# Kernel tuning notes

Hardware: AMD Instinct MI355X
Metric: run time of the kernel (lower is better)

The kernel has to match this reference:

```python
import jax, jax.numpy as jnp
import numpy as np

E, T, D, H = 4, 4096, 2048, 8192

def setup_inputs() -> dict:
    key = jax.random.key(0)
    k1, k2, k3 = jax.random.split(key, 3)
    x = jax.random.normal(k1, (E, T, D), dtype=jnp.float32)
    fc1_w = jax.random.normal(k2, (E, D, H), dtype=jnp.float32) * 0.001
    fc2_w = jax.random.normal(k3, (E, H, D), dtype=jnp.float32) * 0.001
    fc1_b = jnp.zeros((E, 1, H), dtype=jnp.float32)
    fc2_b = jnp.zeros((E, 1, D), dtype=jnp.float32)
    return {"x": x, "fc1_w": fc1_w, "fc1_b": fc1_b, "fc2_w": fc2_w, "fc2_b": fc2_b}

def reference(x, fc1_w, fc1_b, fc2_w, fc2_b):
    # batched expert FFN: y = relu(x @ W1 + b1) @ W2 + b2, per expert e
    y = jnp.einsum('etd,edh->eth', x, fc1_w) + fc1_b
    y = jax.nn.relu(y)
    y = jnp.einsum('eth,ehd->etd', y, fc2_w) + fc2_b
    return y
```

## Files before the change

kernel.cpp:

```cpp
#include <hip/hip_runtime.h>
#include <hip/hip_bf16.h>
#include <stdint.h>

#define E_ 4
#define T_ 4096
#define D_ 2048
#define H_ 8192

typedef __attribute__((ext_vector_type(8))) short bf16x8;
typedef __attribute__((ext_vector_type(4))) float f32x4;
typedef __attribute__((ext_vector_type(4))) unsigned short u16x4;

__device__ __forceinline__ unsigned short f2bf(float f) {
    unsigned int u = __float_as_uint(f);
    u = u + 0x7fffu + ((u >> 16) & 1u);
    return (unsigned short)(u >> 16);
}

__device__ __forceinline__ void async16(const unsigned short* g, unsigned short* l) {
    auto gp = (const __attribute__((address_space(1))) unsigned int*)g;
    auto lp = (__attribute__((address_space(3))) unsigned int*)l;
    __builtin_amdgcn_global_load_lds(gp, lp, 16, 0, 0);
}

__device__ __forceinline__ f32x4 mfma16(bf16x8 a, bf16x8 b, f32x4 c) {
    return __builtin_amdgcn_mfma_f32_16x16x32_bf16(a, b, c, 0, 0, 0);
}

__global__ void cvt_x_kernel(const float4* __restrict__ in, uint2* __restrict__ out, long n4) {
    long i = (long)blockIdx.x * blockDim.x + threadIdx.x;
    long stride = (long)gridDim.x * blockDim.x;
    for (; i < n4; i += stride) {
        float4 v = in[i];
        uint2 o;
        o.x = (unsigned)f2bf(v.x) | ((unsigned)f2bf(v.y) << 16);
        o.y = (unsigned)f2bf(v.z) | ((unsigned)f2bf(v.w) << 16);
        out[i] = o;
    }
}

__global__ void transpose_cvt_kernel(const float* __restrict__ W, unsigned short* __restrict__ Wt,
                                     int R, int C) {
    __shared__ float tile[64][65];
    const float* Wp = W + (size_t)blockIdx.z * R * C;
    unsigned short* Wtp = Wt + (size_t)blockIdx.z * R * C;
    const int c0 = blockIdx.x * 64, r0 = blockIdx.y * 64;
    const int tc = threadIdx.x & 63;
    const int tr = threadIdx.x >> 6;
#pragma unroll
    for (int i = 0; i < 16; ++i) {
        int r = tr * 16 + i;
        tile[r][tc] = Wp[(size_t)(r0 + r) * C + c0 + tc];
    }
    __syncthreads();
#pragma unroll
    for (int i = 0; i < 16; ++i) {
        int r = tr * 16 + i;
        Wtp[(size_t)(c0 + r) * R + r0 + tc] = f2bf(tile[tc][r]);
    }
}

template <int K, int OUT_MODE>
__global__ __launch_bounds__(512, 2) void gemm256_kernel(
    const unsigned short* __restrict__ A,
    const unsigned short* __restrict__ Bt,
    const float* __restrict__ bias,
    void* __restrict__ Cout,
    int M, int N)
{
    constexpr int BK = 64;
    constexpr int NT = K / BK;
    __shared__ __align__(16) unsigned short L[2][2][2][128][64];

    const int nx = gridDim.x, ny = gridDim.y;
    const int nwg = nx * ny * gridDim.z;
    const int w = (blockIdx.z * ny + blockIdx.y) * nx + blockIdx.x;
    const int cpx = nwg >> 3;
    const int xcd = w & 7;
    const int c = w >> 3;
    const int CR = cpx / nx;
    const int GX = (nx % 16 == 0) ? 16 : nx;
    const int g = c / (GX * CR);
    const int r1 = c - g * (GX * CR);
    const int byl = r1 / GX;
    const int bxi = r1 - byl * GX;
    const int fy = xcd * CR + byl;
    const int bx = g * GX + bxi;
    const int e = fy / ny;
    const int by = fy - e * ny;

    const unsigned short* Ae = A + (size_t)e * M * K;
    const unsigned short* Be = Bt + (size_t)e * N * K;
    const int bm0 = by * 256;
    const int bn0 = bx * 256;

    const int tid = threadIdx.x;
    const int lane = tid & 63;
    const int wid = tid >> 6;
    const int wr = wid >> 2;
    const int wc = wid & 3;

    const int srow8 = wid * 8 + (lane >> 3);
    const int skel = 8 * ((lane & 7) ^ (lane >> 3));
    const unsigned short* Abase = Ae + (size_t)(bm0 + srow8) * K + skel;
    const unsigned short* Bbase = Be + (size_t)(bn0 + srow8) * K + skel;

#define STG_A(S_, T_, H_, RO_) \
    async16(Abase + ((size_t)((H_) * 128 + (RO_)) * K + (T_) * BK), \
            &L[S_][0][H_][(RO_) + wid * 8][0])
#define STG_B(S_, T_, H_, RO_) \
    async16(Bbase + ((size_t)((H_) * 128 + (RO_)) * K + (T_) * BK), \
            &L[S_][1][H_][(RO_) + wid * 8][0])

    const int fr = lane & 15;
    const int kq = lane >> 4;
    const int ksw = (lane & 7) << 3;
    const int bh = wc >> 1;
    const int brb = (wc & 1) * 64;

#define RD_A(S_, MOFF_) \
    _Pragma("unroll") for (int m = 0; m < 4; ++m) \
    _Pragma("unroll") for (int kk = 0; kk < 2; ++kk) \
        a[m][kk] = *(const bf16x8*)&L[S_][0][wr][(m + (MOFF_)) * 16 + fr][(kk * 32 + kq * 8) ^ ksw]
#define RD_B(S_, N0_, N1_) \
    _Pragma("unroll") for (int n = (N0_); n < (N1_); ++n) \
    _Pragma("unroll") for (int kk = 0; kk < 2; ++kk) \
        b[n][kk] = *(const bf16x8*)&L[S_][1][bh][brb + n * 16 + fr][(kk * 32 + kq * 8) ^ ksw]

#define MIDBAR do { __builtin_amdgcn_sched_barrier(0); __builtin_amdgcn_s_barrier(); } while (0)
#define CLOSEBAR do { __builtin_amdgcn_s_barrier(); __builtin_amdgcn_sched_barrier(0); } while (0)
#define MFMA_Q(MB_, NB_) do { __builtin_amdgcn_s_setprio(1); \
    _Pragma("unroll") for (int m = 0; m < 4; ++m) \
    _Pragma("unroll") for (int n = 0; n < 2; ++n) \
    _Pragma("unroll") for (int kk = 0; kk < 2; ++kk) \
        acc[(MB_) + m][(NB_) + n] = mfma16(a[m][kk], b[(NB_) + n][kk], acc[(MB_) + m][(NB_) + n]); \
    __builtin_amdgcn_s_setprio(0); } while (0)

    f32x4 acc[8][4] = {};
    bf16x8 a[4][2], b[4][2];

    STG_A(0, 0, 0, 0);  STG_A(0, 0, 1, 0);
    STG_B(0, 0, 0, 0);  STG_B(0, 0, 0, 64);
    STG_B(0, 0, 1, 0);  STG_B(0, 0, 1, 64);
    STG_A(0, 0, 0, 64); STG_A(0, 0, 1, 64);
    STG_A(1, 1, 0, 0);  STG_A(1, 1, 1, 0);
    STG_B(1, 1, 0, 0);  STG_B(1, 1, 0, 64);
    STG_B(1, 1, 1, 0);  STG_B(1, 1, 1, 64);
    asm volatile("s_waitcnt vmcnt(6)" ::: "memory");
    __builtin_amdgcn_sched_barrier(0);
    __builtin_amdgcn_s_barrier();

#define ITER(NOTLAST_) do { \
        const int tA = 2 * j, tB = tA + 1; \
         \
        RD_B(0, 0, 2); RD_A(0, 0); \
        STG_A(1, tB, 0, 64); STG_A(1, tB, 1, 64); \
        MIDBAR; MFMA_Q(0, 0); CLOSEBAR; \
         \
        RD_B(0, 2, 4); \
        if (NOTLAST_) { STG_A(0, tA + 2, 0, 0); STG_A(0, tA + 2, 1, 0); } \
        MIDBAR; MFMA_Q(0, 2); CLOSEBAR; \
         \
        RD_A(0, 4); \
        if (NOTLAST_) { STG_B(0, tA + 2, 0, 0); STG_B(0, tA + 2, 0, 64); } \
        MIDBAR; MFMA_Q(4, 0); CLOSEBAR; \
         \
        if (NOTLAST_) { STG_B(0, tA + 2, 1, 0); STG_B(0, tA + 2, 1, 64); } \
        MIDBAR; MFMA_Q(4, 2); \
        if (NOTLAST_) { asm volatile("s_waitcnt vmcnt(6)" ::: "memory"); } \
        else         { asm volatile("s_waitcnt vmcnt(0)" ::: "memory"); } \
        __builtin_amdgcn_sched_barrier(0); \
        CLOSEBAR; \
         \
        RD_B(1, 0, 2); RD_A(1, 0); \
        if (NOTLAST_) { STG_A(0, tA + 2, 0, 64); STG_A(0, tA + 2, 1, 64); } \
        MIDBAR; MFMA_Q(0, 0); CLOSEBAR; \
         \
        RD_B(1, 2, 4); \
        if (NOTLAST_) { STG_A(1, tB + 2, 0, 0); STG_A(1, tB + 2, 1, 0); } \
        MIDBAR; MFMA_Q(0, 2); CLOSEBAR; \
         \
        RD_A(1, 4); \
        if (NOTLAST_) { STG_B(1, tB + 2, 0, 0); STG_B(1, tB + 2, 0, 64); } \
        MIDBAR; MFMA_Q(4, 0); CLOSEBAR; \
         \
        if (NOTLAST_) { STG_B(1, tB + 2, 1, 0); STG_B(1, tB + 2, 1, 64); } \
        MIDBAR; MFMA_Q(4, 2); \
        if (NOTLAST_) { asm volatile("s_waitcnt vmcnt(6)" ::: "memory"); } \
        else         { asm volatile("s_waitcnt vmcnt(0)" ::: "memory"); } \
        __builtin_amdgcn_sched_barrier(0); \
        CLOSEBAR; \
    } while (0)

    for (int j = 0; j < NT / 2 - 1; ++j) { ITER(true); }
    { const int j = NT / 2 - 1; ITER(false); }

#undef ITER
#undef MFMA_Q
#undef MIDBAR
#undef CLOSEBAR
#undef RD_A
#undef RD_B
#undef STG_A
#undef STG_B

    constexpr int ST = 260;
    float* S = (float*)&L[0][0][0][0][0];
    const int rowq = (lane >> 4) * 4;
    const float* bp = bias + (size_t)e * N;
    const float4 bb4 = *(const float4*)(bp + bn0 + lane * 4);

    unsigned short* Y = (unsigned short*)Cout + (size_t)e * M * N;
    float* O = (float*)Cout + (size_t)e * M * N;

#pragma unroll
    for (int sg = 0; sg < 8; ++sg) {
        __syncthreads();
        if (wr == (sg >> 2)) {
            const int sl = sg & 3;
#pragma unroll
            for (int mm = 0; mm < 2; ++mm) {
#pragma unroll
                for (int n = 0; n < 4; ++n) {
#pragma unroll
                    for (int j2 = 0; j2 < 4; ++j2) {
                        S[(mm * 16 + rowq + j2) * ST + wc * 64 + n * 16 + fr] =
                            acc[2 * sl + mm][n][j2];
                    }
                }
            }
        }
        __syncthreads();
#pragma unroll
        for (int rr = 0; rr < 4; ++rr) {
            const int rl = wid * 4 + rr;
            const int rg = bm0 + sg * 32 + rl;
            f32x4 v = *(const f32x4*)&S[rl * ST + lane * 4];
            v[0] += bb4.x; v[1] += bb4.y; v[2] += bb4.z; v[3] += bb4.w;
            if (OUT_MODE == 0) {
                u16x4 o;
                o[0] = f2bf(fmaxf(v[0], 0.0f));
                o[1] = f2bf(fmaxf(v[1], 0.0f));
                o[2] = f2bf(fmaxf(v[2], 0.0f));
                o[3] = f2bf(fmaxf(v[3], 0.0f));
                *(u16x4*)(Y + (size_t)rg * N + bn0 + lane * 4) = o;
            } else {
                *(f32x4*)(O + (size_t)rg * N + bn0 + lane * 4) = v;
            }
        }
    }
}

extern "C" void kernel_launch(void* const* d_in, const int* in_sizes, int n_in,
                              void* d_out, int out_size, void* d_ws, size_t ws_size,
                              hipStream_t stream) {
    const float* x     = (const float*)d_in[0];
    const float* fc1_w = (const float*)d_in[1];
    const float* fc1_b = (const float*)d_in[2];
    const float* fc2_w = (const float*)d_in[3];
    const float* fc2_b = (const float*)d_in[4];
    float* out = (float*)d_out;

    const size_t n_x  = (size_t)E_ * T_ * D_;
    const size_t n_w1 = (size_t)E_ * D_ * H_;
    const size_t n_w2 = (size_t)E_ * H_ * D_;
    const size_t n_y1 = (size_t)E_ * T_ * H_;

    const size_t need = (n_x + n_w1 + n_w2 + n_y1) * sizeof(unsigned short);
    if (ws_size < need) return;

    unsigned short* xb  = (unsigned short*)d_ws;
    unsigned short* w1t = xb + n_x;
    unsigned short* w2t = w1t + n_w1;
    unsigned short* y1  = w2t + n_w2;

    cvt_x_kernel<<<2048, 256, 0, stream>>>((const float4*)x, (uint2*)xb, (long)(n_x / 4));
    {
        dim3 g(H_ / 64, D_ / 64, E_);
        transpose_cvt_kernel<<<g, 256, 0, stream>>>(fc1_w, w1t, D_, H_);
    }
    {
        dim3 g(D_ / 64, H_ / 64, E_);
        transpose_cvt_kernel<<<g, 256, 0, stream>>>(fc2_w, w2t, H_, D_);
    }
    {
        dim3 g(H_ / 256, T_ / 256, E_);
        gemm256_kernel<D_, 0><<<g, 512, 0, stream>>>(xb, w1t, fc1_b, (void*)y1, T_, H_);
    }
    {
        dim3 g(D_ / 256, T_ / 256, E_);
        gemm256_kernel<H_, 1><<<g, 512, 0, stream>>>(y1, w2t, fc2_b, (void*)out, T_, D_);
    }
}
```

Measured before the change: 1.128 ms.

## Remove mid-phase barriers and overlap LDS fragment reads with MFMA phases

Drops the barrier that sat between each phase's LDS reads and its MFMA block, keeping only the closing barrier. The next phase's B or A fragment reads are moved to run alongside the current MFMA quarter, with the first B read hoisted before the loop. This halves the workgroup barriers per phase and hides LDS latency behind matrix math. The cost is more registers for the fragments and a tighter correctness dependence on barrier placement, since fragment reads now happen right after the vmcnt wait before the closing barrier.

```diff
diff --git a/kernel.cpp b/kernel.cpp
--- a/kernel.cpp
+++ b/kernel.cpp
@@ -127,7 +127,6 @@
     _Pragma("unroll") for (int kk = 0; kk < 2; ++kk) \
         b[n][kk] = *(const bf16x8*)&L[S_][1][bh][brb + n * 16 + fr][(kk * 32 + kq * 8) ^ ksw]
 
-#define MIDBAR do { __builtin_amdgcn_sched_barrier(0); __builtin_amdgcn_s_barrier(); } while (0)
 #define CLOSEBAR do { __builtin_amdgcn_s_barrier(); __builtin_amdgcn_sched_barrier(0); } while (0)
 #define MFMA_Q(MB_, NB_) do { __builtin_amdgcn_s_setprio(1); \
     _Pragma("unroll") for (int m = 0; m < 4; ++m) \
@@ -149,46 +148,61 @@
     asm volatile("s_waitcnt vmcnt(6)" ::: "memory");
     __builtin_amdgcn_sched_barrier(0);
     __builtin_amdgcn_s_barrier();
+    RD_B(0, 0, 2);
 
 #define ITER(NOTLAST_) do { \
         const int tA = 2 * j, tB = tA + 1; \
          \
-        RD_B(0, 0, 2); RD_A(0, 0); \
+        RD_A(0, 0); \
         STG_A(1, tB, 0, 64); STG_A(1, tB, 1, 64); \
-        MIDBAR; MFMA_Q(0, 0); CLOSEBAR; \
-         \
+        __builtin_amdgcn_sched_barrier(0); \
+        MFMA_Q(0, 0); \
         RD_B(0, 2, 4); \
+        CLOSEBAR; \
+         \
         if (NOTLAST_) { STG_A(0, tA + 2, 0, 0); STG_A(0, tA + 2, 1, 0); } \
-        MIDBAR; MFMA_Q(0, 2); CLOSEBAR; \
-         \
+        __builtin_amdgcn_sched_barrier(0); \
+        MFMA_Q(0, 2); \
         RD_A(0, 4); \
+        CLOSEBAR; \
+         \
         if (NOTLAST_) { STG_B(0, tA + 2, 0, 0); STG_B(0, tA + 2, 0, 64); } \
-        MIDBAR; MFMA_Q(4, 0); CLOSEBAR; \
+        __builtin_amdgcn_sched_barrier(0); \
+        MFMA_Q(4, 0); \
+        CLOSEBAR; \
          \
         if (NOTLAST_) { STG_B(0, tA + 2, 1, 0); STG_B(0, tA + 2, 1, 64); } \
-        MIDBAR; MFMA_Q(4, 2); \
         if (NOTLAST_) { asm volatile("s_waitcnt vmcnt(6)" ::: "memory"); } \
         else         { asm volatile("s_waitcnt vmcnt(0)" ::: "memory"); } \
         __builtin_amdgcn_sched_barrier(0); \
-        CLOSEBAR; \
-         \
-        RD_B(1, 0, 2); RD_A(1, 0); \
+        RD_B(1, 0, 2); \
+        MFMA_Q(4, 2); \
+        CLOSEBAR; \
+         \
+        RD_A(1, 0); \
         if (NOTLAST_) { STG_A(0, tA + 2, 0, 64); STG_A(0, tA + 2, 1, 64); } \
-        MIDBAR; MFMA_Q(0, 0); CLOSEBAR; \
-         \
+        __builtin_amdgcn_sched_barrier(0); \
+        MFMA_Q(0, 0); \
         RD_B(1, 2, 4); \
+        CLOSEBAR; \
+         \
         if (NOTLAST_) { STG_A(1, tB + 2, 0, 0); STG_A(1, tB + 2, 1, 0); } \
-        MIDBAR; MFMA_Q(0, 2); CLOSEBAR; \
-         \
+        __builtin_amdgcn_sched_barrier(0); \
+        MFMA_Q(0, 2); \
         RD_A(1, 4); \
+        CLOSEBAR; \
+         \
         if (NOTLAST_) { STG_B(1, tB + 2, 0, 0); STG_B(1, tB + 2, 0, 64); } \
-        MIDBAR; MFMA_Q(4, 0); CLOSEBAR; \
+        __builtin_amdgcn_sched_barrier(0); \
+        MFMA_Q(4, 0); \
+        CLOSEBAR; \
          \
         if (NOTLAST_) { STG_B(1, tB + 2, 1, 0); STG_B(1, tB + 2, 1, 64); } \
-        MIDBAR; MFMA_Q(4, 2); \
         if (NOTLAST_) { asm volatile("s_waitcnt vmcnt(6)" ::: "memory"); } \
         else         { asm volatile("s_waitcnt vmcnt(0)" ::: "memory"); } \
         __builtin_amdgcn_sched_barrier(0); \
+        if (NOTLAST_) { RD_B(0, 0, 2); } \
+        MFMA_Q(4, 2); \
         CLOSEBAR; \
     } while (0)
 
@@ -197,7 +211,6 @@
 
 #undef ITER
 #undef MFMA_Q
-#undef MIDBAR
 #undef CLOSEBAR
 #undef RD_A
 #undef RD_B
```

Result: faster. 1.076 ms (-4.6%).

## Collapse GEMM main loop into two-phase-per-tile schedule with fewer barriers

Applied to the files above, without the earlier changes.

Replaces the eight quarter-phase loop body (16 block barriers per two K-tiles) with two half-phases per tile. Each half-phase issues a full 4x4 MFMA block while the LDS fragments for the next half or next tile are read. All loads for tile T+2 are issued together before the second half. The aim is to cut barrier and s_waitcnt stalls and to overlap LDS reads with MFMA work. In exchange, more A/B fragments and in-flight loads stay live at once, which raises register pressure, and the deeper interleaving carries a risk of LDS read/write hazards.

```diff
diff --git a/kernel.cpp b/kernel.cpp
--- a/kernel.cpp
+++ b/kernel.cpp
@@ -122,18 +122,17 @@
     _Pragma("unroll") for (int m = 0; m < 4; ++m) \
     _Pragma("unroll") for (int kk = 0; kk < 2; ++kk) \
         a[m][kk] = *(const bf16x8*)&L[S_][0][wr][(m + (MOFF_)) * 16 + fr][(kk * 32 + kq * 8) ^ ksw]
-#define RD_B(S_, N0_, N1_) \
-    _Pragma("unroll") for (int n = (N0_); n < (N1_); ++n) \
+#define RD_B(S_) \
+    _Pragma("unroll") for (int n = 0; n < 4; ++n) \
     _Pragma("unroll") for (int kk = 0; kk < 2; ++kk) \
         b[n][kk] = *(const bf16x8*)&L[S_][1][bh][brb + n * 16 + fr][(kk * 32 + kq * 8) ^ ksw]
 
-#define MIDBAR do { __builtin_amdgcn_sched_barrier(0); __builtin_amdgcn_s_barrier(); } while (0)
 #define CLOSEBAR do { __builtin_amdgcn_s_barrier(); __builtin_amdgcn_sched_barrier(0); } while (0)
-#define MFMA_Q(MB_, NB_) do { __builtin_amdgcn_s_setprio(1); \
+#define MFMA_H(MB_) do { __builtin_amdgcn_s_setprio(1); \
     _Pragma("unroll") for (int m = 0; m < 4; ++m) \
-    _Pragma("unroll") for (int n = 0; n < 2; ++n) \
+    _Pragma("unroll") for (int n = 0; n < 4; ++n) \
     _Pragma("unroll") for (int kk = 0; kk < 2; ++kk) \
-        acc[(MB_) + m][(NB_) + n] = mfma16(a[m][kk], b[(NB_) + n][kk], acc[(MB_) + m][(NB_) + n]); \
+        acc[(MB_) + m][n] = mfma16(a[m][kk], b[n][kk], acc[(MB_) + m][n]); \
     __builtin_amdgcn_s_setprio(0); } while (0)
 
     f32x4 acc[8][4] = {};
@@ -149,55 +148,49 @@
     asm volatile("s_waitcnt vmcnt(6)" ::: "memory");
     __builtin_amdgcn_sched_barrier(0);
     __builtin_amdgcn_s_barrier();
-
-#define ITER(NOTLAST_) do { \
-        const int tA = 2 * j, tB = tA + 1; \
-         \
-        RD_B(0, 0, 2); RD_A(0, 0); \
-        STG_A(1, tB, 0, 64); STG_A(1, tB, 1, 64); \
-        MIDBAR; MFMA_Q(0, 0); CLOSEBAR; \
-         \
-        RD_B(0, 2, 4); \
-        if (NOTLAST_) { STG_A(0, tA + 2, 0, 0); STG_A(0, tA + 2, 1, 0); } \
-        MIDBAR; MFMA_Q(0, 2); CLOSEBAR; \
-         \
-        RD_A(0, 4); \
-        if (NOTLAST_) { STG_B(0, tA + 2, 0, 0); STG_B(0, tA + 2, 0, 64); } \
-        MIDBAR; MFMA_Q(4, 0); CLOSEBAR; \
-         \
-        if (NOTLAST_) { STG_B(0, tA + 2, 1, 0); STG_B(0, tA + 2, 1, 64); } \
-        MIDBAR; MFMA_Q(4, 2); \
-        if (NOTLAST_) { asm volatile("s_waitcnt vmcnt(6)" ::: "memory"); } \
-        else         { asm volatile("s_waitcnt vmcnt(0)" ::: "memory"); } \
+    RD_B(0);
+    RD_A(0, 0);
+
+#define PH_A(T_, S_, HAS_NEXT_) do { \
+        if (HAS_NEXT_) { STG_A((S_) ^ 1, (T_) + 1, 0, 64); STG_A((S_) ^ 1, (T_) + 1, 1, 64); } \
         __builtin_amdgcn_sched_barrier(0); \
-        CLOSEBAR; \
-         \
-        RD_B(1, 0, 2); RD_A(1, 0); \
-        if (NOTLAST_) { STG_A(0, tA + 2, 0, 64); STG_A(0, tA + 2, 1, 64); } \
-        MIDBAR; MFMA_Q(0, 0); CLOSEBAR; \
-         \
-        RD_B(1, 2, 4); \
-        if (NOTLAST_) { STG_A(1, tB + 2, 0, 0); STG_A(1, tB + 2, 1, 0); } \
-        MIDBAR; MFMA_Q(0, 2); CLOSEBAR; \
-         \
-        RD_A(1, 4); \
-        if (NOTLAST_) { STG_B(1, tB + 2, 0, 0); STG_B(1, tB + 2, 0, 64); } \
-        MIDBAR; MFMA_Q(4, 0); CLOSEBAR; \
-         \
-        if (NOTLAST_) { STG_B(1, tB + 2, 1, 0); STG_B(1, tB + 2, 1, 64); } \
-        MIDBAR; MFMA_Q(4, 2); \
-        if (NOTLAST_) { asm volatile("s_waitcnt vmcnt(6)" ::: "memory"); } \
-        else         { asm volatile("s_waitcnt vmcnt(0)" ::: "memory"); } \
-        __builtin_amdgcn_sched_barrier(0); \
+        MFMA_H(0); \
+        RD_A(S_, 4); \
         CLOSEBAR; \
     } while (0)
 
-    for (int j = 0; j < NT / 2 - 1; ++j) { ITER(true); }
-    { const int j = NT / 2 - 1; ITER(false); }
-
-#undef ITER
-#undef MFMA_Q
-#undef MIDBAR
+#define PH_B(T_, S_, HAS_NEXT_, HAS_NEXT2_) do { \
+        if (HAS_NEXT2_) { \
+            STG_A(S_, (T_) + 2, 0, 0);  STG_A(S_, (T_) + 2, 1, 0); \
+            STG_B(S_, (T_) + 2, 0, 0);  STG_B(S_, (T_) + 2, 0, 64); \
+            STG_B(S_, (T_) + 2, 1, 0);  STG_B(S_, (T_) + 2, 1, 64); \
+        } \
+        if (HAS_NEXT2_) { asm volatile("s_waitcnt vmcnt(6)" ::: "memory"); } \
+        else            { asm volatile("s_waitcnt vmcnt(0)" ::: "memory"); } \
+        __builtin_amdgcn_sched_barrier(0); \
+        MFMA_H(4); \
+        if (HAS_NEXT_) { RD_B((S_) ^ 1); RD_A((S_) ^ 1, 0); } \
+        CLOSEBAR; \
+    } while (0)
+
+    for (int j = 0; j < NT / 2 - 1; ++j) {
+        const int tA = 2 * j, tB = tA + 1;
+        PH_A(tA, 0, true);
+        PH_B(tA, 0, true, (tA + 2 < NT));
+        PH_A(tB, 1, (tB + 1 < NT));
+        PH_B(tB, 1, (tB + 1 < NT), (tB + 2 < NT));
+    }
+    {
+        const int tA = NT - 2, tB = NT - 1;
+        PH_A(tA, 0, true);
+        PH_B(tA, 0, true, false);
+        PH_A(tB, 1, false);
+        PH_B(tB, 1, false, false);
+    }
+
+#undef PH_A
+#undef PH_B
+#undef MFMA_H
 #undef CLOSEBAR
 #undef RD_A
 #undef RD_B
```

After: 1.108 ms. Within noise of the previous version (-1.8%).
